# Kernel optimization log

Measured on AMD Instinct MI355X. Metric: run time of the kernel, lower is better.

## Reference

```python
import jax, jax.numpy as jnp
import numpy as np

NUM_HEADS = 12

def setup_inputs() -> dict:
    key = jax.random.key(0)
    k1, k2, k3 = jax.random.split(key, 3)
    B, T, H = 2, 2048, 768
    x = jax.random.normal(k1, (B, T, H), dtype=jnp.float32)
    attn_mask = jnp.ones((B, T), dtype=jnp.int32)
    Wqkv = jax.random.normal(k2, (H, 3 * H), dtype=jnp.float32) * 0.02
    bqkv = jnp.zeros((3 * H,), dtype=jnp.float32)
    Wproj = jax.random.normal(k3, (H, H), dtype=jnp.float32) * 0.02
    bproj = jnp.zeros((H,), dtype=jnp.float32)
    return {"x": x, "attn_mask": attn_mask, "Wqkv": Wqkv, "bqkv": bqkv,
            "Wproj": Wproj, "bproj": bproj}

def reference(x, attn_mask, Wqkv, bqkv, Wproj, bproj):
    B, T, H = x.shape
    nh = NUM_HEADS
    hd = H // nh
    qkv = x @ Wqkv + bqkv                      # [B,T,3H]
    q, k, v = jnp.split(qkv, 3, axis=-1)
    # [B,T,H] -> [B,nh,T,hd]
    def heads(t):
        return t.reshape(B, T, nh, hd).transpose(0, 2, 1, 3)
    q, k, v = heads(q), heads(k), heads(v)
    scores = jnp.einsum('bhqd,bhkd->bhqk', q, k) / jnp.sqrt(jnp.float32(hd))
    causal = jnp.tril(jnp.ones((T, T), dtype=bool))          # allowed positions
    key_ok = attn_mask.astype(bool)[:, None, None, :]        # [B,1,1,T]
    allowed = causal[None, None] & key_ok
    scores = jnp.where(allowed, scores, -jnp.inf)
    weights = jax.nn.softmax(scores, axis=-1)                # dropout=0 (eval)
    out = jnp.einsum('bhqk,bhkd->bhqd', weights, v)
    out = out.transpose(0, 2, 1, 3).reshape(B, T, H)
    return out @ Wproj + bproj
```

## Files before the change

### kernel.cpp

```cpp
#include <hip/hip_runtime.h>
#include <stdint.h>

typedef unsigned short u16;
typedef unsigned int   u32;
typedef unsigned char  u8;
typedef __attribute__((ext_vector_type(8))) short short8;
typedef __attribute__((ext_vector_type(4))) float f32x4;
typedef __attribute__((ext_vector_type(4))) unsigned short u16x4;

#define DEV static __device__ __forceinline__

static constexpr int Bc = 2, Tc = 2048, Hc = 768, NH = 12, HD = 64;
static constexpr int BTc = Bc * Tc;
static constexpr int N3 = 3 * Hc;
static constexpr int NBH = Bc * NH;
static constexpr int NITEMS = 32 * NBH;
static constexpr float QSCALE = 0.125f * 1.44269504088896f;
static constexpr float MRINIT = -1.0e38f;
static constexpr float SMASK  = -3.0e38f;

DEV u16 f2bf(float f) {
  u32 u = __float_as_uint(f);
  u32 r = (u + 0x7fffu + ((u >> 16) & 1u)) >> 16;
  return (u16)r;
}

DEV float fexp2(float x) {
#if __has_builtin(__builtin_amdgcn_exp2f)
  return __builtin_amdgcn_exp2f(x);
#else
  return exp2f(x);
#endif
}

DEV u32 cvtpk_bf16(float lo, float hi) {
  u32 r;
  asm("v_cvt_pk_bf16_f32 %0, %1, %2" : "=v"(r) : "v"(lo), "v"(hi));
  return r;
}

DEV void gl_lds16(const u16* g, u16* l) {
  __builtin_amdgcn_global_load_lds(
      (const __attribute__((address_space(1))) u32*)g,
      (__attribute__((address_space(3))) u32*)l, 16, 0, 0);
}

#define MFMA(a, b, c) __builtin_amdgcn_mfma_f32_16x16x32_bf16((a), (b), (c), 0, 0, 0)

__global__ void k_cvt(const float4* __restrict__ in, uint4* __restrict__ out, int n8,
                      const int* __restrict__ mask, u8* __restrict__ flags,
                      u32* __restrict__ ctr) {
  if (blockIdx.x == 0 && threadIdx.x < 64) {
    int t = threadIdx.x;
    if (t == 0) *ctr = 0;
    int b = t >> 5, kb = t & 31;
    const int* m = mask + b * Tc + kb * 64;
    int all = 1;
    for (int i = 0; i < 64; ++i) all &= (m[i] != 0);
    flags[b * 32 + kb] = (u8)all;
  }
  int i = blockIdx.x * 256 + threadIdx.x;
  if (i >= n8) return;
  float4 a = in[2 * i], b = in[2 * i + 1];
  uint4 o;
  o.x = f2bf(a.x) | ((u32)f2bf(a.y) << 16);
  o.y = f2bf(a.z) | ((u32)f2bf(a.w) << 16);
  o.z = f2bf(b.x) | ((u32)f2bf(b.y) << 16);
  o.w = f2bf(b.z) | ((u32)f2bf(b.w) << 16);
  out[i] = o;
}

__global__ __launch_bounds__(256) void k_transpose_w2(const float* __restrict__ Wqkv,
                                                      const float* __restrict__ Wproj,
                                                      u16* __restrict__ WqkvT,
                                                      u16* __restrict__ WprojT) {
  __shared__ u16 tile[64][65];
  int y = blockIdx.y, x = blockIdx.x;
  const float* in; u16* out; int R, C, r0, c0;
  if (y < 12) { in = Wqkv; out = WqkvT; R = Hc; C = N3; r0 = y * 64; c0 = x * 64; }
  else {
    if (x >= 12) return;
    in = Wproj; out = WprojT; R = Hc; C = Hc; r0 = (y - 12) * 64; c0 = x * 64;
  }
  int tx = threadIdx.x, ty = threadIdx.y;
  for (int i = ty; i < 64; i += 4)
    tile[i][tx] = f2bf(in[(size_t)(r0 + i) * C + c0 + tx]);
  __syncthreads();
  for (int i = ty; i < 64; i += 4)
    out[(size_t)(c0 + i) * R + r0 + tx] = tile[tx][i];
}

template <int EPI>
__global__ __launch_bounds__(256) void k_gemm(const u16* __restrict__ A,
                                              const u16* __restrict__ BTm,
                                              const float* __restrict__ bias,
                                              u16* __restrict__ oQ, u16* __restrict__ oK,
                                              u16* __restrict__ oV, float* __restrict__ oF,
                                              int M, int N, int K) {
  __shared__ u16 As[128 * 32];
  __shared__ u16 Bs[128 * 32];
  const int tid = threadIdx.x;
  const int lane = tid & 63, wave = tid >> 6;
  const int wr = wave >> 1, wc = wave & 1;
  const int row0 = blockIdx.y * 128, col0 = blockIdx.x * 128;

  f32x4 acc[4][4];
#pragma unroll
  for (int m = 0; m < 4; ++m)
#pragma unroll
    for (int n = 0; n < 4; ++n) acc[m][n] = (f32x4)(0.f);

  const int srow = lane >> 2;
  const int sg = lane & 3;
  const int sf = (lane >> 3) & 3;
  const int kfetch = ((sg ^ sf) * 8);

  const int r16 = lane & 15;
  const int g = lane >> 4;
  const int fr = (r16 >> 1) & 3;
  const int koff = ((g ^ fr) * 8);

  for (int k0 = 0; k0 < K; k0 += 32) {
    if (k0) __syncthreads();
#pragma unroll
    for (int p = 0; p < 2; ++p) {
      int seg = wave * 2 + p;
      int row = seg * 16 + srow;
      gl_lds16(A + (size_t)(row0 + row) * K + k0 + kfetch, &As[seg * 512 + lane * 8]);
      gl_lds16(BTm + (size_t)(col0 + row) * K + k0 + kfetch, &Bs[seg * 512 + lane * 8]);
    }
    __syncthreads();
    short8 af[4], bf[4];
#pragma unroll
    for (int m = 0; m < 4; ++m)
      af[m] = *(const short8*)&As[(wr * 64 + m * 16 + r16) * 32 + koff];
#pragma unroll
    for (int n = 0; n < 4; ++n)
      bf[n] = *(const short8*)&Bs[(wc * 64 + n * 16 + r16) * 32 + koff];
#pragma unroll
    for (int m = 0; m < 4; ++m)
#pragma unroll
      for (int n = 0; n < 4; ++n)
        acc[m][n] = MFMA(af[m], bf[n], acc[m][n]);
  }

#pragma unroll
  for (int m = 0; m < 4; ++m) {
    int rowg = row0 + wr * 64 + m * 16 + g * 4;
#pragma unroll
    for (int n = 0; n < 4; ++n) {
      int colg = col0 + wc * 64 + n * 16 + r16;
      float bv = bias[colg];
      if constexpr (EPI == 0) {
        int which = colg / Hc;
        int hc = colg - which * Hc;
        int h = hc >> 6, d = hc & 63;
        int b = rowg >> 11, t0 = rowg & 2047;
        if (which == 2) {
          u16x4 pk;
#pragma unroll
          for (int r = 0; r < 4; ++r) pk[r] = f2bf(acc[m][n][r] + bv);
          *(u16x4*)&oV[((size_t)(b * NH + h) * HD + d) * Tc + t0] = pk;
        } else {
#pragma unroll
          for (int r = 0; r < 4; ++r) {
            float v = acc[m][n][r] + bv;
            size_t dst = ((size_t)(b * NH + h) * Tc + t0 + r) * HD + d;
            if (which == 0) oQ[dst] = f2bf(v * QSCALE);
            else            oK[dst] = f2bf(v);
          }
        }
      } else {
#pragma unroll
        for (int r = 0; r < 4; ++r)
          oF[(size_t)(rowg + r) * Hc + colg] = acc[m][n][r] + bv;
      }
    }
  }
}

__global__ __launch_bounds__(512, 4) void k_attn(const u16* __restrict__ Qh,
                                                 const u16* __restrict__ Kh,
                                                 const u16* __restrict__ VT,
                                                 const int* __restrict__ mask,
                                                 const u8* __restrict__ flags,
                                                 u16* __restrict__ O,
                                                 u32* __restrict__ ctr) {
  __shared__ u16 Ks[2][8192];
  __shared__ u16 Vs[2][8192];
  __shared__ u16 Ps[8][1024];
  int* s_item = (int*)&Ps[1][0];
  float* ml = (float*)&Ps[0][0];
  const int tid = threadIdx.x, lane = tid & 63, wave = tid >> 6;
  const int qgrp = wave >> 1;
  const int kh = wave & 1;
  const int r16 = lane & 15, g = lane >> 4;
  const int r7 = r16 & 7;
  const int skey = lane >> 3;
  const int sgr = lane & 7;
  const int sgd = ((sgr ^ skey) * 8);

  const int off0 = r16 * 64 + ((g ^ r7) * 8);
  const int off1 = r16 * 64 + (((4 + g) ^ r7) * 8);
  const int vo0 = r16 * 128 + (kh * 8 + (g ^ r7)) * 8;
  const int vo1 = r16 * 128 + (kh * 8 + ((4 + g) ^ r7)) * 8;

  for (;;) {
    if (tid == 0) *s_item = (int)atomicAdd(ctr, 1u);
    __syncthreads();
    const int item = *s_item;
    if (item >= NITEMS) break;
    const int qt = 31 - item / NBH;
    const int bh = item % NBH;
    const int b = bh / NH, h = bh - b * NH;
    const int q0 = qt * 64;
    const int nt = qt / 2 + 1;
    const int qg = q0 + qgrp * 16 + r16;
    const int* mrow = mask + b * Tc;
    const u8* frow = flags + b * 32;

    const u16* qbase = Qh + ((size_t)bh * Tc + qg) * HD;
    const short8 qf0 = *(const short8*)(qbase + g * 8);
    const short8 qf1 = *(const short8*)(qbase + 32 + g * 8);

    f32x4 acc[4];
#pragma unroll
    for (int n = 0; n < 4; ++n) acc[n] = (f32x4)(0.f);
    float mrun = MRINIT, lrun = 0.f;

    auto stage = [&](int slot, int kb) {
#pragma unroll
      for (int p = 0; p < 2; ++p) {
        int seg = 2 * wave + p;
        int rloc = 8 * seg + skey;
        gl_lds16(Kh + ((size_t)bh * Tc + kb + rloc) * HD + sgd,
                 &Ks[slot][seg * 512 + lane * 8]);
      }
#pragma unroll
      for (int p = 0; p < 2; ++p) {
        int dloc = 8 * wave + 4 * p + g;
        int vsg = (((r16 & 8) | ((r16 & 7) ^ (dloc & 7)))) * 8;
        gl_lds16(VT + ((size_t)bh * HD + dloc) * Tc + kb + vsg,
                 &Vs[slot][wave * 1024 + p * 512 + lane * 8]);
      }
    };

    stage(0, 0);

    for (int t = 0; t < nt; ++t) {
      const int kb = t * 128;

      asm volatile("s_waitcnt vmcnt(0)" ::: "memory");
      __builtin_amdgcn_sched_barrier(0);
      __builtin_amdgcn_s_barrier();
      __builtin_amdgcn_sched_barrier(0);

      if (t + 1 < nt) stage((t + 1) & 1, kb + 128);

      const u16* Kc = &Ks[t & 1][0];
      const u16* Vc = &Vs[t & 1][0];

      const int kbw = kb + 64 * kh;
      const bool dead = (kbw > q0 + 63);
      if (!dead) {
        f32x4 s[4];
        __builtin_amdgcn_s_setprio(1);
#pragma unroll
        for (int nn = 0; nn < 4; ++nn) {
          const int ng = 4 * kh + nn;
          short8 kf0 = *(const short8*)&Kc[ng * 1024 + off0];
          short8 kf1 = *(const short8*)&Kc[ng * 1024 + off1];
          f32x4 z = (f32x4)(0.f);
          z = MFMA(kf0, qf0, z);
          z = MFMA(kf1, qf1, z);
          s[nn] = z;
        }
        __builtin_amdgcn_s_setprio(0);

        const bool diag = (kbw == q0);
        if (diag || !frow[2 * t + kh]) {
          const int fl = frow[2 * t + kh];
#pragma unroll
          for (int nn = 0; nn < 4; ++nn)
#pragma unroll
            for (int r = 0; r < 4; ++r) {
              int keyg = kbw + 16 * nn + 4 * g + r;
              bool ok = fl ? true : (mrow[keyg] != 0);
              if (diag) ok = ok && (keyg <= qg);
              if (!ok) s[nn][r] = SMASK;
            }
        }

        float lm;
        {
          float m0 = fmaxf(fmaxf(s[0][0], s[0][1]), fmaxf(s[0][2], s[0][3]));
          float m1 = fmaxf(fmaxf(s[1][0], s[1][1]), fmaxf(s[1][2], s[1][3]));
          float m2 = fmaxf(fmaxf(s[2][0], s[2][1]), fmaxf(s[2][2], s[2][3]));
          float m3 = fmaxf(fmaxf(s[3][0], s[3][1]), fmaxf(s[3][2], s[3][3]));
          lm = fmaxf(fmaxf(m0, m1), fmaxf(m2, m3));
        }
        if (!__all(lm <= mrun + 8.0f)) {
          float rm = fmaxf(lm, __shfl_xor(lm, 16));
          rm = fmaxf(rm, __shfl_xor(rm, 32));
          float nm = fmaxf(mrun, rm);
          float alpha = fexp2(mrun - nm);
          mrun = nm;
          lrun *= alpha;
#pragma unroll
          for (int r = 0; r < 4; ++r) {
            float ar = __shfl(alpha, g * 4 + r);
            acc[0][r] *= ar;
            acc[1][r] *= ar;
            acc[2][r] *= ar;
            acc[3][r] *= ar;
          }
        }
        float rs = 0.f;
#pragma unroll
        for (int nn = 0; nn < 4; ++nn)
#pragma unroll
          for (int r = 0; r < 4; ++r) {
            float p = fexp2(s[nn][r] - mrun);
            s[nn][r] = p;
            rs += p;
          }
        lrun += rs;

        u32* pw = (u32*)&Ps[wave][0];
#pragma unroll
        for (int nn = 0; nn < 4; ++nn) {
          u32 lo = cvtpk_bf16(s[nn][0], s[nn][1]);
          u32 hi = cvtpk_bf16(s[nn][2], s[nn][3]);
          int idx = r16 * 32 + (((2 * nn + (g >> 1)) ^ r7) << 2) + 2 * (g & 1);
          *(uint2*)&pw[idx] = make_uint2(lo, hi);
        }
        const u16* pr = &Ps[wave][0];
        short8 pa0 = *(const short8*)&pr[off0];
        short8 pa1 = *(const short8*)&pr[off1];

        __builtin_amdgcn_s_setprio(1);
#pragma unroll
        for (int n = 0; n < 4; ++n) {
          short8 vf0 = *(const short8*)&Vc[n * 2048 + vo0];
          short8 vf1 = *(const short8*)&Vc[n * 2048 + vo1];
          acc[n] = MFMA(pa0, vf0, acc[n]);
          acc[n] = MFMA(pa1, vf1, acc[n]);
        }
        __builtin_amdgcn_s_setprio(0);
      }
      __builtin_amdgcn_sched_barrier(0);
    }

    float lt = lrun + __shfl_xor(lrun, 16);
    lt += __shfl_xor(lt, 32);

    __syncthreads();
    float* ab = (float*)&Ks[0][0] + qgrp * 1024;
    if (kh == 1) {
#pragma unroll
      for (int n = 0; n < 4; ++n)
#pragma unroll
        for (int r = 0; r < 4; ++r)
          ab[(4 * g + r) * 64 + 16 * n + r16] = acc[n][r];
      if (g == 0) {
        ml[qgrp * 32 + r16 * 2]     = mrun;
        ml[qgrp * 32 + r16 * 2 + 1] = lt;
      }
    }
    __syncthreads();
    if (kh == 0) {
#pragma unroll
      for (int r = 0; r < 4; ++r) {
        int q = 4 * g + r;
        float mA = __shfl(mrun, q);
        float lA = __shfl(lt, q);
        float mB = ml[qgrp * 32 + q * 2];
        float lB = ml[qgrp * 32 + q * 2 + 1];
        float ms = fmaxf(mA, mB);
        float cA = fexp2(mA - ms);
        float cB = fexp2(mB - ms);
        float linv = 1.0f / (lA * cA + lB * cB);
        int qr = q0 + qgrp * 16 + q;
        u16* orow = O + ((size_t)(b * Tc + qr)) * Hc + h * 64;
#pragma unroll
        for (int n = 0; n < 4; ++n) {
          float v = (acc[n][r] * cA + ab[q * 64 + 16 * n + r16] * cB) * linv;
          orow[n * 16 + r16] = f2bf(v);
        }
      }
    }
  }
}

extern "C" void kernel_launch(void* const* d_in, const int* in_sizes, int n_in,
                              void* d_out, int out_size, void* d_ws, size_t ws_size,
                              hipStream_t stream) {
  const float* x = (const float*)d_in[0];
  const int* mask = (const int*)d_in[1];
  const float* Wqkv = (const float*)d_in[2];
  const float* bqkv = (const float*)d_in[3];
  const float* Wproj = (const float*)d_in[4];
  const float* bproj = (const float*)d_in[5];
  float* out = (float*)d_out;

  char* ws = (char*)d_ws;
  size_t off = 0;
  auto alloc = [&](size_t bytes) {
    char* p = ws + off;
    off += (bytes + 255) & ~(size_t)255;
    return p;
  };
  u16* xb     = (u16*)alloc((size_t)BTc * Hc * 2);
  u16* WqkvT  = (u16*)alloc((size_t)N3 * Hc * 2);
  u16* WprojT = (u16*)alloc((size_t)Hc * Hc * 2);
  u16* Qh     = (u16*)alloc((size_t)BTc * Hc * 2);
  u16* Kh     = (u16*)alloc((size_t)BTc * Hc * 2);
  u16* VT     = (u16*)alloc((size_t)BTc * Hc * 2);
  u32* ctr    = (u32*)alloc(256);
  u8*  flags  = (u8*)alloc(256);
  u16* Ob     = xb;

  int n8 = BTc * Hc / 8;
  k_cvt<<<(n8 + 255) / 256, 256, 0, stream>>>((const float4*)x, (uint4*)xb, n8,
                                              mask, flags, ctr);
  k_transpose_w2<<<dim3(36, 24), dim3(64, 4), 0, stream>>>(Wqkv, Wproj, WqkvT, WprojT);
  k_gemm<0><<<dim3(N3 / 128, BTc / 128), 256, 0, stream>>>(xb, WqkvT, bqkv, Qh, Kh, VT,
                                                           nullptr, BTc, N3, Hc);
  k_attn<<<dim3(512), 512, 0, stream>>>(Qh, Kh, VT, mask, flags, Ob, ctr);
  k_gemm<1><<<dim3(Hc / 128, BTc / 128), 256, 0, stream>>>(Ob, WprojT, bproj, nullptr,
                                                           nullptr, nullptr, out, BTc, Hc, Hc);
}
```

Measured before the change: 100.3 us.

## Restructure attention waves into 2 query groups by 4 key splits with register-resident P

Reorganizes the attention kernel so each wave handles 32 query rows (two 16-row halves sharing K/V fragments) over a 32-key slice, with four key-split waves per query group instead of two. The V layout written by the QKV GEMM epilogue is permuted so that the softmax probabilities can feed the PV MFMA directly from registers, removing the per-wave LDS round trip for P. The final merge combines four partial accumulators through swizzled shared memory and writes 16-byte vectorized outputs. This trades more registers and a larger 4-way merge for better K/V fragment reuse and fewer LDS operations.

```diff
diff --git a/kernel.cpp b/kernel.cpp
--- a/kernel.cpp
+++ b/kernel.cpp
@@ -7,6 +7,7 @@
 typedef __attribute__((ext_vector_type(8))) short short8;
 typedef __attribute__((ext_vector_type(4))) float f32x4;
 typedef __attribute__((ext_vector_type(4))) unsigned short u16x4;
+typedef __attribute__((ext_vector_type(4))) unsigned int u32x4;
 
 #define DEV static __device__ __forceinline__
 
@@ -157,10 +158,12 @@
         int h = hc >> 6, d = hc & 63;
         int b = rowg >> 11, t0 = rowg & 2047;
         if (which == 2) {
+          int o = t0 & 31;
+          int t0p = (t0 & ~31) | (((o >> 2) & 3) * 8 + ((o >> 4) & 1) * 4);
           u16x4 pk;
 #pragma unroll
           for (int r = 0; r < 4; ++r) pk[r] = f2bf(acc[m][n][r] + bv);
-          *(u16x4*)&oV[((size_t)(b * NH + h) * HD + d) * Tc + t0] = pk;
+          *(u16x4*)&oV[((size_t)(b * NH + h) * HD + d) * Tc + t0p] = pk;
         } else {
 #pragma unroll
           for (int r = 0; r < 4; ++r) {
@@ -186,62 +189,68 @@
                                                  const u8* __restrict__ flags,
                                                  u16* __restrict__ O,
                                                  u32* __restrict__ ctr) {
-  __shared__ u16 Ks[2][8192];
-  __shared__ u16 Vs[2][8192];
-  __shared__ u16 Ps[8][1024];
-  int* s_item = (int*)&Ps[1][0];
-  float* ml = (float*)&Ps[0][0];
+  __shared__ u16 SM[32768];
+  __shared__ float mlbuf[512];
+  __shared__ int s_item;
+  u16* Ksp = SM;
+  u16* Vsp = SM + 16384;
+
   const int tid = threadIdx.x, lane = tid & 63, wave = tid >> 6;
-  const int qgrp = wave >> 1;
-  const int kh = wave & 1;
+  const int qgrp = wave >> 2;
+  const int kq = wave & 3;
   const int r16 = lane & 15, g = lane >> 4;
   const int r7 = r16 & 7;
-  const int skey = lane >> 3;
-  const int sgr = lane & 7;
+  const int skey = lane >> 3, sgr = lane & 7;
   const int sgd = ((sgr ^ skey) * 8);
 
   const int off0 = r16 * 64 + ((g ^ r7) * 8);
   const int off1 = r16 * 64 + (((4 + g) ^ r7) * 8);
-  const int vo0 = r16 * 128 + (kh * 8 + (g ^ r7)) * 8;
-  const int vo1 = r16 * 128 + (kh * 8 + ((4 + g) ^ r7)) * 8;
+  const int gi = 4 * kq + g;
+  const int voff = r16 * 128 + (((gi & 8) | ((gi & 7) ^ r7)) * 8);
 
   for (;;) {
-    if (tid == 0) *s_item = (int)atomicAdd(ctr, 1u);
+    if (tid == 0) s_item = (int)atomicAdd(ctr, 1u);
     __syncthreads();
-    const int item = *s_item;
+    const int item = s_item;
     if (item >= NITEMS) break;
     const int qt = 31 - item / NBH;
     const int bh = item % NBH;
     const int b = bh / NH, h = bh - b * NH;
     const int q0 = qt * 64;
     const int nt = qt / 2 + 1;
-    const int qg = q0 + qgrp * 16 + r16;
+    const int ql0 = q0 + 32 * qgrp;
+    const int qlane = ql0 + r16;
     const int* mrow = mask + b * Tc;
     const u8* frow = flags + b * 32;
 
-    const u16* qbase = Qh + ((size_t)bh * Tc + qg) * HD;
-    const short8 qf0 = *(const short8*)(qbase + g * 8);
-    const short8 qf1 = *(const short8*)(qbase + 32 + g * 8);
-
-    f32x4 acc[4];
-#pragma unroll
-    for (int n = 0; n < 4; ++n) acc[n] = (f32x4)(0.f);
-    float mrun = MRINIT, lrun = 0.f;
+    const u16* qbase = Qh + ((size_t)bh * Tc + qlane) * HD;
+    const short8 qfA0 = *(const short8*)(qbase + g * 8);
+    const short8 qfA1 = *(const short8*)(qbase + 32 + g * 8);
+    const short8 qfB0 = *(const short8*)(qbase + 16 * HD + g * 8);
+    const short8 qfB1 = *(const short8*)(qbase + 16 * HD + 32 + g * 8);
+
+    f32x4 accL[4], accH[4];
+#pragma unroll
+    for (int n = 0; n < 4; ++n) { accL[n] = (f32x4)(0.f); accH[n] = (f32x4)(0.f); }
+    float mL = MRINIT, mH = MRINIT, lL = 0.f, lH = 0.f;
+
+    const u16* kgb = Kh + (size_t)bh * Tc * HD;
+    const u16* vgb = VT + (size_t)bh * HD * Tc;
 
     auto stage = [&](int slot, int kb) {
+      u16* kd = Ksp + slot * 8192;
+      u16* vd = Vsp + slot * 8192;
 #pragma unroll
       for (int p = 0; p < 2; ++p) {
         int seg = 2 * wave + p;
         int rloc = 8 * seg + skey;
-        gl_lds16(Kh + ((size_t)bh * Tc + kb + rloc) * HD + sgd,
-                 &Ks[slot][seg * 512 + lane * 8]);
+        gl_lds16(kgb + (size_t)(kb + rloc) * HD + sgd, kd + seg * 512 + lane * 8);
       }
 #pragma unroll
       for (int p = 0; p < 2; ++p) {
         int dloc = 8 * wave + 4 * p + g;
         int vsg = (((r16 & 8) | ((r16 & 7) ^ (dloc & 7)))) * 8;
-        gl_lds16(VT + ((size_t)bh * HD + dloc) * Tc + kb + vsg,
-                 &Vs[slot][wave * 1024 + p * 512 + lane * 8]);
+        gl_lds16(vgb + (size_t)dloc * Tc + kb + vsg, vd + wave * 1024 + p * 512 + lane * 8);
       }
     };
 
@@ -249,145 +258,152 @@
 
     for (int t = 0; t < nt; ++t) {
       const int kb = t * 128;
-
       asm volatile("s_waitcnt vmcnt(0)" ::: "memory");
       __builtin_amdgcn_sched_barrier(0);
       __builtin_amdgcn_s_barrier();
       __builtin_amdgcn_sched_barrier(0);
-
       if (t + 1 < nt) stage((t + 1) & 1, kb + 128);
 
-      const u16* Kc = &Ks[t & 1][0];
-      const u16* Vc = &Vs[t & 1][0];
-
-      const int kbw = kb + 64 * kh;
-      const bool dead = (kbw > q0 + 63);
-      if (!dead) {
-        f32x4 s[4];
-        __builtin_amdgcn_s_setprio(1);
-#pragma unroll
-        for (int nn = 0; nn < 4; ++nn) {
-          const int ng = 4 * kh + nn;
-          short8 kf0 = *(const short8*)&Kc[ng * 1024 + off0];
-          short8 kf1 = *(const short8*)&Kc[ng * 1024 + off1];
-          f32x4 z = (f32x4)(0.f);
-          z = MFMA(kf0, qf0, z);
-          z = MFMA(kf1, qf1, z);
-          s[nn] = z;
+      const int kbw = kb + 32 * kq;
+      if (kbw > ql0 + 31) { __builtin_amdgcn_sched_barrier(0); continue; }
+
+      const u16* Kc = Ksp + (t & 1) * 8192;
+      const u16* Vc = Vsp + (t & 1) * 8192;
+
+      f32x4 sL[2], sH[2];
+      __builtin_amdgcn_s_setprio(1);
+#pragma unroll
+      for (int ng = 0; ng < 2; ++ng) {
+        const int NG = 2 * kq + ng;
+        short8 kf0 = *(const short8*)&Kc[NG * 1024 + off0];
+        short8 kf1 = *(const short8*)&Kc[NG * 1024 + off1];
+        f32x4 zl = (f32x4)(0.f), zh = (f32x4)(0.f);
+        zl = MFMA(kf0, qfA0, zl); zl = MFMA(kf1, qfA1, zl);
+        zh = MFMA(kf0, qfB0, zh); zh = MFMA(kf1, qfB1, zh);
+        sL[ng] = zl; sH[ng] = zh;
+      }
+      __builtin_amdgcn_s_setprio(0);
+
+      const int fl = frow[2 * t + (kq >> 1)];
+      const bool allok = (kbw + 31 <= ql0) && fl;
+      if (!allok) {
+#pragma unroll
+        for (int ng = 0; ng < 2; ++ng)
+#pragma unroll
+          for (int r = 0; r < 4; ++r) {
+            int keyg = kbw + 16 * ng + 4 * g + r;
+            bool okc = fl ? true : (mrow[keyg] != 0);
+            if (!(okc && keyg <= qlane))      sL[ng][r] = SMASK;
+            if (!(okc && keyg <= qlane + 16)) sH[ng][r] = SMASK;
+          }
+      }
+
+      float lmL, lmH;
+      {
+        float a0 = fmaxf(fmaxf(sL[0][0], sL[0][1]), fmaxf(sL[0][2], sL[0][3]));
+        float a1 = fmaxf(fmaxf(sL[1][0], sL[1][1]), fmaxf(sL[1][2], sL[1][3]));
+        lmL = fmaxf(a0, a1);
+        float b0 = fmaxf(fmaxf(sH[0][0], sH[0][1]), fmaxf(sH[0][2], sH[0][3]));
+        float b1 = fmaxf(fmaxf(sH[1][0], sH[1][1]), fmaxf(sH[1][2], sH[1][3]));
+        lmH = fmaxf(b0, b1);
+      }
+      bool okd = (lmL <= mL + 8.0f) && (lmH <= mH + 8.0f);
+      if (!__all(okd)) {
+        float rmL = fmaxf(lmL, __shfl_xor(lmL, 16)); rmL = fmaxf(rmL, __shfl_xor(rmL, 32));
+        float rmH = fmaxf(lmH, __shfl_xor(lmH, 16)); rmH = fmaxf(rmH, __shfl_xor(rmH, 32));
+        float nmL = fmaxf(mL, rmL), nmH = fmaxf(mH, rmH);
+        float aL = fexp2(mL - nmL), aH = fexp2(mH - nmH);
+        mL = nmL; mH = nmH; lL *= aL; lH *= aH;
+#pragma unroll
+        for (int r = 0; r < 4; ++r) {
+          float arL = __shfl(aL, g * 4 + r);
+          float arH = __shfl(aH, g * 4 + r);
+          accL[0][r] *= arL; accL[1][r] *= arL; accL[2][r] *= arL; accL[3][r] *= arL;
+          accH[0][r] *= arH; accH[1][r] *= arH; accH[2][r] *= arH; accH[3][r] *= arH;
         }
-        __builtin_amdgcn_s_setprio(0);
-
-        const bool diag = (kbw == q0);
-        if (diag || !frow[2 * t + kh]) {
-          const int fl = frow[2 * t + kh];
-#pragma unroll
-          for (int nn = 0; nn < 4; ++nn)
-#pragma unroll
-            for (int r = 0; r < 4; ++r) {
-              int keyg = kbw + 16 * nn + 4 * g + r;
-              bool ok = fl ? true : (mrow[keyg] != 0);
-              if (diag) ok = ok && (keyg <= qg);
-              if (!ok) s[nn][r] = SMASK;
-            }
+      }
+      float rsL = 0.f, rsH = 0.f;
+#pragma unroll
+      for (int ng = 0; ng < 2; ++ng)
+#pragma unroll
+        for (int r = 0; r < 4; ++r) {
+          float pL = fexp2(sL[ng][r] - mL); sL[ng][r] = pL; rsL += pL;
+          float pH = fexp2(sH[ng][r] - mH); sH[ng][r] = pH; rsH += pH;
         }
-
-        float lm;
-        {
-          float m0 = fmaxf(fmaxf(s[0][0], s[0][1]), fmaxf(s[0][2], s[0][3]));
-          float m1 = fmaxf(fmaxf(s[1][0], s[1][1]), fmaxf(s[1][2], s[1][3]));
-          float m2 = fmaxf(fmaxf(s[2][0], s[2][1]), fmaxf(s[2][2], s[2][3]));
-          float m3 = fmaxf(fmaxf(s[3][0], s[3][1]), fmaxf(s[3][2], s[3][3]));
-          lm = fmaxf(fmaxf(m0, m1), fmaxf(m2, m3));
-        }
-        if (!__all(lm <= mrun + 8.0f)) {
-          float rm = fmaxf(lm, __shfl_xor(lm, 16));
-          rm = fmaxf(rm, __shfl_xor(rm, 32));
-          float nm = fmaxf(mrun, rm);
-          float alpha = fexp2(mrun - nm);
-          mrun = nm;
-          lrun *= alpha;
-#pragma unroll
-          for (int r = 0; r < 4; ++r) {
-            float ar = __shfl(alpha, g * 4 + r);
-            acc[0][r] *= ar;
-            acc[1][r] *= ar;
-            acc[2][r] *= ar;
-            acc[3][r] *= ar;
-          }
-        }
-        float rs = 0.f;
-#pragma unroll
-        for (int nn = 0; nn < 4; ++nn)
-#pragma unroll
-          for (int r = 0; r < 4; ++r) {
-            float p = fexp2(s[nn][r] - mrun);
-            s[nn][r] = p;
-            rs += p;
-          }
-        lrun += rs;
-
-        u32* pw = (u32*)&Ps[wave][0];
-#pragma unroll
-        for (int nn = 0; nn < 4; ++nn) {
-          u32 lo = cvtpk_bf16(s[nn][0], s[nn][1]);
-          u32 hi = cvtpk_bf16(s[nn][2], s[nn][3]);
-          int idx = r16 * 32 + (((2 * nn + (g >> 1)) ^ r7) << 2) + 2 * (g & 1);
-          *(uint2*)&pw[idx] = make_uint2(lo, hi);
-        }
-        const u16* pr = &Ps[wave][0];
-        short8 pa0 = *(const short8*)&pr[off0];
-        short8 pa1 = *(const short8*)&pr[off1];
-
-        __builtin_amdgcn_s_setprio(1);
-#pragma unroll
-        for (int n = 0; n < 4; ++n) {
-          short8 vf0 = *(const short8*)&Vc[n * 2048 + vo0];
-          short8 vf1 = *(const short8*)&Vc[n * 2048 + vo1];
-          acc[n] = MFMA(pa0, vf0, acc[n]);
-          acc[n] = MFMA(pa1, vf1, acc[n]);
-        }
-        __builtin_amdgcn_s_setprio(0);
-      }
+      lL += rsL; lH += rsH;
+
+      u32x4 PL, PH;
+      PL[0] = cvtpk_bf16(sL[0][0], sL[0][1]); PL[1] = cvtpk_bf16(sL[0][2], sL[0][3]);
+      PL[2] = cvtpk_bf16(sL[1][0], sL[1][1]); PL[3] = cvtpk_bf16(sL[1][2], sL[1][3]);
+      PH[0] = cvtpk_bf16(sH[0][0], sH[0][1]); PH[1] = cvtpk_bf16(sH[0][2], sH[0][3]);
+      PH[2] = cvtpk_bf16(sH[1][0], sH[1][1]); PH[3] = cvtpk_bf16(sH[1][2], sH[1][3]);
+      short8 paL = __builtin_bit_cast(short8, PL);
+      short8 paH = __builtin_bit_cast(short8, PH);
+
+      __builtin_amdgcn_s_setprio(1);
+#pragma unroll
+      for (int n = 0; n < 4; ++n) {
+        short8 vf = *(const short8*)&Vc[n * 2048 + voff];
+        accL[n] = MFMA(paL, vf, accL[n]);
+        accH[n] = MFMA(paH, vf, accH[n]);
+      }
+      __builtin_amdgcn_s_setprio(0);
       __builtin_amdgcn_sched_barrier(0);
     }
 
-    float lt = lrun + __shfl_xor(lrun, 16);
-    lt += __shfl_xor(lt, 32);
+    float ltL = lL + __shfl_xor(lL, 16); ltL += __shfl_xor(ltL, 32);
+    float ltH = lH + __shfl_xor(lH, 16); ltH += __shfl_xor(ltH, 32);
 
     __syncthreads();
-    float* ab = (float*)&Ks[0][0] + qgrp * 1024;
-    if (kh == 1) {
+    float* part = (float*)SM;
+    {
+      float* pb = part + (size_t)(qgrp * 4 + kq) * 2048;
 #pragma unroll
       for (int n = 0; n < 4; ++n)
 #pragma unroll
-        for (int r = 0; r < 4; ++r)
-          ab[(4 * g + r) * 64 + 16 * n + r16] = acc[n][r];
+        for (int r = 0; r < 4; ++r) {
+          int c = 16 * n + r16;
+          pb[(4 * g + r) * 64 + (c ^ (g * 8))] = accL[n][r];
+          pb[(16 + 4 * g + r) * 64 + (c ^ ((4 + g) * 8))] = accH[n][r];
+        }
       if (g == 0) {
-        ml[qgrp * 32 + r16 * 2]     = mrun;
-        ml[qgrp * 32 + r16 * 2 + 1] = lt;
+        float* mb = mlbuf + (qgrp * 4 + kq) * 64;
+        mb[2 * r16] = mL;            mb[2 * r16 + 1] = ltL;
+        mb[2 * (16 + r16)] = mH;     mb[2 * (16 + r16) + 1] = ltH;
       }
     }
     __syncthreads();
-    if (kh == 0) {
-#pragma unroll
-      for (int r = 0; r < 4; ++r) {
-        int q = 4 * g + r;
-        float mA = __shfl(mrun, q);
-        float lA = __shfl(lt, q);
-        float mB = ml[qgrp * 32 + q * 2];
-        float lB = ml[qgrp * 32 + q * 2 + 1];
-        float ms = fmaxf(mA, mB);
-        float cA = fexp2(mA - ms);
-        float cB = fexp2(mB - ms);
-        float linv = 1.0f / (lA * cA + lB * cB);
-        int qr = q0 + qgrp * 16 + q;
-        u16* orow = O + ((size_t)(b * Tc + qr)) * Hc + h * 64;
-#pragma unroll
-        for (int n = 0; n < 4; ++n) {
-          float v = (acc[n][r] * cA + ab[q * 64 + 16 * n + r16] * cB) * linv;
-          orow[n * 16 + r16] = f2bf(v);
-        }
-      }
+    {
+      int R = wave * 8 + (lane >> 3);
+      int qgv = R >> 5, q32 = R & 31;
+      int dp = (lane & 7) * 8;
+      int dps = dp ^ (((q32 >> 2) & 7) * 8);
+      const float* mb = mlbuf + qgv * 256;
+      float m0 = mb[0 * 64 + 2 * q32], l0 = mb[0 * 64 + 2 * q32 + 1];
+      float m1 = mb[1 * 64 + 2 * q32], l1 = mb[1 * 64 + 2 * q32 + 1];
+      float m2 = mb[2 * 64 + 2 * q32], l2 = mb[2 * 64 + 2 * q32 + 1];
+      float m3 = mb[3 * 64 + 2 * q32], l3 = mb[3 * 64 + 2 * q32 + 1];
+      float ms = fmaxf(fmaxf(m0, m1), fmaxf(m2, m3));
+      float c0 = fexp2(m0 - ms), c1 = fexp2(m1 - ms);
+      float c2 = fexp2(m2 - ms), c3 = fexp2(m3 - ms);
+      float inv = 1.0f / (c0 * l0 + c1 * l1 + c2 * l2 + c3 * l3);
+      const float* p0 = part + (size_t)(qgv * 4 + 0) * 2048 + q32 * 64 + dps;
+      const float* p1 = p0 + 2048, *p2 = p0 + 4096, *p3 = p0 + 6144;
+      f32x4 aA = *(const f32x4*)p0, aB = *(const f32x4*)(p0 + 4);
+      f32x4 bA = *(const f32x4*)p1, bB = *(const f32x4*)(p1 + 4);
+      f32x4 cA = *(const f32x4*)p2, cB = *(const f32x4*)(p2 + 4);
+      f32x4 dA = *(const f32x4*)p3, dB = *(const f32x4*)(p3 + 4);
+      float o[8];
+#pragma unroll
+      for (int j = 0; j < 4; ++j) {
+        o[j]     = (c0 * aA[j] + c1 * bA[j] + c2 * cA[j] + c3 * dA[j]) * inv;
+        o[4 + j] = (c0 * aB[j] + c1 * bB[j] + c2 * cB[j] + c3 * dB[j]) * inv;
+      }
+      u32x4 W;
+      W[0] = cvtpk_bf16(o[0], o[1]); W[1] = cvtpk_bf16(o[2], o[3]);
+      W[2] = cvtpk_bf16(o[4], o[5]); W[3] = cvtpk_bf16(o[6], o[7]);
+      *(short8*)(O + ((size_t)(b * Tc + q0 + R)) * Hc + h * 64 + dp) =
+          __builtin_bit_cast(short8, W);
     }
   }
 }
```

New measurement: 104.5 us. 1.04x slower.
